# Kernel optimization log

Hardware: AMD Instinct MI355X
Metric: run time of the kernel (lower is better)

The kernel has to match this reference:

```python
import jax, jax.numpy as jnp
import numpy as np

EMBD = 512
HEADS = 8
HEAD = EMBD // HEADS


def setup_inputs() -> dict:
    key = jax.random.key(0)
    ks = jax.random.split(key, 9)
    B, M = 4, 2048
    s = 1.0 / np.sqrt(EMBD)
    inp = {
        "x": jax.random.normal(ks[0], (B, M, EMBD), dtype=jnp.float32),
        "wq": jax.random.uniform(ks[1], (EMBD, EMBD), jnp.float32, -s, s),
        "bq": jnp.zeros((EMBD,), jnp.float32),
        "wk": jax.random.uniform(ks[2], (EMBD, EMBD), jnp.float32, -s, s),
        "bk": jnp.zeros((EMBD,), jnp.float32),
        "wv": jax.random.uniform(ks[3], (EMBD, EMBD), jnp.float32, -s, s),
        "bv": jnp.zeros((EMBD,), jnp.float32),
        "wo": jax.random.uniform(ks[4], (EMBD, EMBD), jnp.float32, -s, s),
        "bo": jnp.zeros((EMBD,), jnp.float32),
        "gamma": jnp.ones((EMBD,), jnp.float32),
        "beta": jnp.zeros((EMBD,), jnp.float32),
    }
    return inp


def layer_norm(x, gamma, beta, eps=1e-5):
    mu = jnp.mean(x, axis=-1, keepdims=True)
    var = jnp.mean(jnp.square(x - mu), axis=-1, keepdims=True)
    return (x - mu) * jax.lax.rsqrt(var + eps) * gamma + beta


def reference(x, wq, bq, wk, bk, wv, bv, wo, bo, gamma, beta):
    B, M, _ = x.shape
    norm = layer_norm(x, gamma, beta)
    # projections; reshape to [B, H, M, Dh]
    def proj(w, b):
        return (norm @ w.T + b).reshape(B, M, HEADS, HEAD).transpose(0, 2, 1, 3)
    q = proj(wq, bq)
    k = proj(wk, bk)
    v = proj(wv, bv)
    scores = jnp.einsum("bhmd,bhnd->bhmn", q, k) / np.sqrt(HEAD)
    # exclude self-attention on the diagonal
    diag = jnp.eye(M, dtype=bool)
    scores = jnp.where(diag, -jnp.inf, scores)
    attn = jax.nn.softmax(scores, axis=-1)
    ctx = jnp.einsum("bhmn,bhnd->bhmd", attn, v)
    ctx = ctx.transpose(0, 2, 1, 3).reshape(B, M, EMBD)
    out = ctx @ wo.T + bo
    return (out + x, attn)
```

## Files before the change

kernel.cpp:

```cpp
#include <hip/hip_runtime.h>

#define B_   4
#define H_   8
#define M_   2048
#define D_   512
#define DH_  64

typedef short  bf16x8 __attribute__((ext_vector_type(8)));
typedef float  f32x4  __attribute__((ext_vector_type(4)));
typedef unsigned short u16x4 __attribute__((ext_vector_type(4)));

#define EXPC 0.18033688011112042f

static __device__ __forceinline__ unsigned short f2bf(float f) {
  unsigned u = __float_as_uint(f);
  u += 0x7fffu + ((u >> 16) & 1u);
  return (unsigned short)(u >> 16);
}

static __device__ __forceinline__ int swz128(int row, int byteoff) {
  return row * 128 + (byteoff ^ ((row & 7) << 4));
}

static __device__ __forceinline__ void glds16(const void* g, void* l) {
  __builtin_amdgcn_global_load_lds(
      (const __attribute__((address_space(1))) unsigned*)g,
      (__attribute__((address_space(3))) unsigned*)l, 16, 0, 0);
}

static __device__ __forceinline__ void stage_tile(
    const char* g0, size_t rstride, char* lds, int t) {
  const int r0 = t >> 3, c0 = t & 7;
  const char* src = g0 + (size_t)r0 * rstride + ((c0 ^ (r0 & 7)) << 4);
  char* dst = lds + ((t & 192) << 4);
  #pragma unroll
  for (int c = 0; c < 4; ++c)
    glds16(src + (size_t)c * 32 * rstride, dst + c * 4096);
}

__global__ __launch_bounds__(256) void ln_kernel(
    const float* __restrict__ x, const float* __restrict__ gamma,
    const float* __restrict__ beta, unsigned short* __restrict__ xn)
{
  int row = blockIdx.x;
  int t = threadIdx.x;
  const float* xr = x + (size_t)row * D_;
  float v0 = xr[t], v1 = xr[t + 256];
  float s = v0 + v1, ss = v0 * v0 + v1 * v1;
  #pragma unroll
  for (int m = 1; m < 64; m <<= 1) {
    s  += __shfl_xor(s, m);
    ss += __shfl_xor(ss, m);
  }
  __shared__ float red[8];
  int wid = t >> 6;
  if ((t & 63) == 0) { red[wid] = s; red[wid + 4] = ss; }
  __syncthreads();
  s  = red[0] + red[1] + red[2] + red[3];
  ss = red[4] + red[5] + red[6] + red[7];
  float mu  = s * (1.0f / D_);
  float var = ss * (1.0f / D_) - mu * mu;
  float rstd = rsqrtf(var + 1e-5f);
  unsigned short* o = xn + (size_t)row * D_;
  o[t]       = f2bf((v0 - mu) * rstd * gamma[t]       + beta[t]);
  o[t + 256] = f2bf((v1 - mu) * rstd * gamma[t + 256] + beta[t + 256]);
}

__global__ __launch_bounds__(256) void cast_w_kernel(
    const float* __restrict__ wq, const float* __restrict__ wk,
    const float* __restrict__ wv, const float* __restrict__ wo,
    unsigned short* __restrict__ wqkv, unsigned short* __restrict__ wob)
{
  int i = blockIdx.x * 256 + threadIdx.x;
  wqkv[i]          = f2bf(wq[i]);
  wqkv[i + 262144] = f2bf(wk[i]);
  wqkv[i + 524288] = f2bf(wv[i]);
  wob[i]           = f2bf(wo[i]);
}

__global__ __launch_bounds__(256) void qkv_gemm(
    const unsigned short* __restrict__ xn,
    const unsigned short* __restrict__ wqkv,
    const float* __restrict__ bq, const float* __restrict__ bk,
    const float* __restrict__ bv,
    unsigned short* __restrict__ q, unsigned short* __restrict__ k,
    unsigned short* __restrict__ vT)
{
  __shared__ __align__(16) char As[128 * 128];
  __shared__ __align__(16) char Bs[128 * 128];
  const int m0 = blockIdx.x * 128;
  const int n0 = blockIdx.y * 128;
  const int t = threadIdx.x, wid = t >> 6, lane = t & 63;
  const int wr = (wid >> 1) * 64, wc = (wid & 1) * 64;
  const int cl = lane & 15, rg = lane >> 4;
  const f32x4 z4 = {0.f, 0.f, 0.f, 0.f};
  const bool isv = (n0 >= 1024);

  const char* agb = (const char*)xn   + (size_t)m0 * 1024;
  const char* bgb = (const char*)wqkv + (size_t)n0 * 1024;

  f32x4 acc[4][4];
  #pragma unroll
  for (int i = 0; i < 4; ++i)
    #pragma unroll
    for (int j = 0; j < 4; ++j) acc[i][j] = z4;

  for (int k0 = 0; k0 < 512; k0 += 64) {
    __syncthreads();
    stage_tile(agb + k0 * 2, 1024, As, t);
    stage_tile(bgb + k0 * 2, 1024, Bs, t);
    __syncthreads();
    #pragma unroll
    for (int ks = 0; ks < 2; ++ks) {
      int koff = ks * 64 + rg * 16;
      bf16x8 af[4], bfr[4];
      #pragma unroll
      for (int i = 0; i < 4; ++i)
        af[i] = *(const bf16x8*)(As + swz128(wr + i * 16 + cl, koff));
      #pragma unroll
      for (int j = 0; j < 4; ++j)
        bfr[j] = *(const bf16x8*)(Bs + swz128(wc + j * 16 + cl, koff));
      if (isv) {
        #pragma unroll
        for (int i = 0; i < 4; ++i)
          #pragma unroll
          for (int j = 0; j < 4; ++j)
            acc[i][j] = __builtin_amdgcn_mfma_f32_16x16x32_bf16(af[i], bfr[j], acc[i][j], 0, 0, 0);
      } else {
        #pragma unroll
        for (int j = 0; j < 4; ++j)
          #pragma unroll
          for (int i = 0; i < 4; ++i)
            acc[j][i] = __builtin_amdgcn_mfma_f32_16x16x32_bf16(bfr[j], af[i], acc[j][i], 0, 0, 0);
      }
    }
  }

  if (isv) {
    #pragma unroll
    for (int j = 0; j < 4; ++j) {
      int n = n0 + wc + j * 16 + cl;
      int nn = n & 511;
      int h = nn >> 6, dh = nn & 63;
      float bias = bv[nn];
      #pragma unroll
      for (int i = 0; i < 4; ++i) {
        int mrow = m0 + wr + i * 16 + rg * 4;
        int b = mrow >> 11, mm = mrow & 2047;
        u16x4 u;
        #pragma unroll
        for (int r = 0; r < 4; ++r) u[r] = f2bf(acc[i][j][r] + bias);
        *(u16x4*)(vT + ((size_t)(b * H_ + h) * DH_ + dh) * M_ + mm) = u;
      }
    }
  } else {
    const int mat = n0 >> 9;
    unsigned short* dst = mat ? k : q;
    const float* bias = mat ? bk : bq;
    #pragma unroll
    for (int j = 0; j < 4; ++j) {
      int nn0 = ((n0 + wc) & 511) + j * 16 + rg * 4;
      int h = nn0 >> 6, dh = nn0 & 63;
      f32x4 b4 = *(const f32x4*)(bias + nn0);
      #pragma unroll
      for (int i = 0; i < 4; ++i) {
        int mrow = m0 + wr + i * 16 + cl;
        int b = mrow >> 11, mm = mrow & 2047;
        u16x4 u;
        #pragma unroll
        for (int r = 0; r < 4; ++r) u[r] = f2bf(acc[j][i][r] + b4[r]);
        *(u16x4*)(dst + ((size_t)(b * H_ + h) * M_ + mm) * DH_ + dh) = u;
      }
    }
  }
}

__global__ __launch_bounds__(256, 8) void psum_kernel(
    const unsigned short* __restrict__ q, const unsigned short* __restrict__ k,
    float* __restrict__ rinv)
{
  __shared__ __align__(16) char Kb[2][8192];
  const int flat = blockIdx.x;
  const int bh = (flat & 7) * 4 + ((flat >> 3) >> 5);
  const int mb = (flat >> 3) & 31;
  const int m0 = mb * 64;
  const int t = threadIdx.x, wid = t >> 6, lane = t & 63;
  const int wr = wid * 16, cl = lane & 15, rg = lane >> 4;
  const char* qb = (const char*)(q + (size_t)bh * M_ * DH_);
  const char* kb = (const char*)(k + (size_t)bh * M_ * DH_);
  const int m_g = m0 + wr + cl;
  const f32x4 z4 = {0.f, 0.f, 0.f, 0.f};

  bf16x8 qf[2];
  #pragma unroll
  for (int ks = 0; ks < 2; ++ks)
    qf[ks] = *(const bf16x8*)(qb + (size_t)m_g * 128 + ks * 64 + rg * 16);

  const int r0 = t >> 3, c0 = t & 7;
  const int ldsoff = (t & 192) * 16;
  const size_t sK0 = (size_t)r0 * 128 + ((c0 ^ (r0 & 7)) << 4);

  glds16(kb + sK0,        Kb[0] + ldsoff);
  glds16(kb + sK0 + 4096, Kb[0] + ldsoff + 4096);

  float psum = 0.f;
  int buf = 0;
  for (int nt = 0; nt < 32; ++nt) {
    __syncthreads();
    if (nt + 1 < 32) {
      const char* src = kb + (size_t)(nt + 1) * 8192;
      glds16(src + sK0,        Kb[buf ^ 1] + ldsoff);
      glds16(src + sK0 + 4096, Kb[buf ^ 1] + ldsoff + 4096);
    }
    f32x4 s[4];
    #pragma unroll
    for (int j = 0; j < 4; ++j) s[j] = z4;
    #pragma unroll
    for (int ks = 0; ks < 2; ++ks)
      #pragma unroll
      for (int j = 0; j < 4; ++j) {
        bf16x8 kf = *(const bf16x8*)(Kb[buf] + swz128(j * 16 + cl, ks * 64 + rg * 16));
        s[j] = __builtin_amdgcn_mfma_f32_16x16x32_bf16(kf, qf[ks], s[j], 0, 0, 0);
      }
    if (nt == mb) {
      #pragma unroll
      for (int j = 0; j < 4; ++j)
        #pragma unroll
        for (int r = 0; r < 4; ++r) {
          int n_g = nt * 64 + j * 16 + rg * 4 + r;
          float p = __builtin_amdgcn_exp2f(s[j][r] * EXPC);
          psum += (n_g == m_g) ? 0.f : p;
        }
    } else {
      #pragma unroll
      for (int j = 0; j < 4; ++j)
        #pragma unroll
        for (int r = 0; r < 4; ++r)
          psum += __builtin_amdgcn_exp2f(s[j][r] * EXPC);
    }
    buf ^= 1;
  }
  psum += __shfl_xor(psum, 16);
  psum += __shfl_xor(psum, 32);
  if (lane < 16) rinv[bh * M_ + m_g] = 1.0f / psum;
}

__global__ __launch_bounds__(256, 4) void attn_kernel(
    const unsigned short* __restrict__ q,
    const unsigned short* __restrict__ k,
    const unsigned short* __restrict__ vT,
    const float* __restrict__ rinv,
    float* __restrict__ attn,
    unsigned short* __restrict__ ctx)
{
  __shared__ __align__(16) char Kb[2][8192];
  __shared__ __align__(16) char Vb[2][8192];
  __shared__ __align__(16) char Ps[4][2048];

  const int flat = blockIdx.x;
  const int bh = (flat & 7) * 4 + ((flat >> 3) >> 5);
  const int mb = (flat >> 3) & 31;
  const int m0 = mb * 64;
  const int t = threadIdx.x, wid = t >> 6, lane = t & 63;
  const int wr = wid * 16, cl = lane & 15, rg = lane >> 4;
  const int m_g = m0 + wr + cl;
  const f32x4 z4 = {0.f, 0.f, 0.f, 0.f};

  const char* qb = (const char*)(q  + (size_t)bh * M_ * DH_);
  const char* kb = (const char*)(k  + (size_t)bh * M_ * DH_);
  const char* vb = (const char*)(vT + (size_t)bh * DH_ * M_);
  float* ab = attn + (size_t)bh * M_ * M_;

  const float rv = rinv[bh * M_ + m_g];
  bf16x8 qf[2];
  #pragma unroll
  for (int ks = 0; ks < 2; ++ks)
    qf[ks] = *(const bf16x8*)(qb + (size_t)m_g * 128 + ks * 64 + rg * 16);

  const int r0 = t >> 3, c0 = t & 7;
  const int ldsoff = (t & 192) * 16;
  const size_t sK0 = (size_t)r0 * 128 + ((c0 ^ (r0 & 7)) << 4);
  const size_t sV0 = (size_t)r0 * (M_ * 2) + ((c0 ^ (r0 & 7)) << 4);

  glds16(kb + sK0,                    Kb[0] + ldsoff);
  glds16(kb + sK0 + 4096,             Kb[0] + ldsoff + 4096);
  glds16(vb + sV0,                    Vb[0] + ldsoff);
  glds16(vb + sV0 + 32 * (M_ * 2),    Vb[0] + ldsoff + 4096);
  __syncthreads();

  f32x4 oc[4];
  #pragma unroll
  for (int j = 0; j < 4; ++j) oc[j] = z4;

  const int srow = lane >> 4;
  const int sch  = lane & 15;

  int buf = 0;
  for (int nt = 0; nt < 32; ++nt) {
    if (nt + 1 < 32) {
      const char* srcK = kb + (size_t)(nt + 1) * 8192;
      const char* srcV = vb + (size_t)(nt + 1) * 128;
      glds16(srcK + sK0,                 Kb[buf ^ 1] + ldsoff);
      glds16(srcK + sK0 + 4096,          Kb[buf ^ 1] + ldsoff + 4096);
      glds16(srcV + sV0,                 Vb[buf ^ 1] + ldsoff);
      glds16(srcV + sV0 + 32 * (M_ * 2), Vb[buf ^ 1] + ldsoff + 4096);
    }
    f32x4 s[4];
    #pragma unroll
    for (int j = 0; j < 4; ++j) s[j] = z4;
    #pragma unroll
    for (int ks = 0; ks < 2; ++ks)
      #pragma unroll
      for (int j = 0; j < 4; ++j) {
        bf16x8 kf = *(const bf16x8*)(Kb[buf] + swz128(j * 16 + cl, ks * 64 + rg * 16));
        s[j] = __builtin_amdgcn_mfma_f32_16x16x32_bf16(kf, qf[ks], s[j], 0, 0, 0);
      }
    const bool dtile = (nt == mb);
    #pragma unroll
    for (int j = 0; j < 4; ++j) {
      u16x4 u;
      #pragma unroll
      for (int r = 0; r < 4; ++r) {
        int n_g = nt * 64 + j * 16 + rg * 4 + r;
        float p = __builtin_amdgcn_exp2f(s[j][r] * EXPC) * rv;
        u[r] = f2bf((dtile && n_g == m_g) ? 0.f : p);
      }
      *(u16x4*)(Ps[wid] + swz128(cl, j * 32 + rg * 8)) = u;
    }
    {
      float* abase = ab + ((size_t)(m0 + wr + srow)) * M_ + nt * 64 + sch * 4;
      #pragma unroll
      for (int it = 0; it < 4; ++it) {
        u16x4 pu = *(const u16x4*)(Ps[wid] + swz128(it * 4 + srow, sch * 8));
        f32x4 pv;
        #pragma unroll
        for (int r = 0; r < 4; ++r) pv[r] = __uint_as_float((unsigned)pu[r] << 16);
        __builtin_nontemporal_store(pv, (f32x4*)(abase + (size_t)it * 4 * M_));
      }
    }
    #pragma unroll
    for (int ks = 0; ks < 2; ++ks) {
      bf16x8 pf = *(const bf16x8*)(Ps[wid] + swz128(cl, ks * 64 + rg * 16));
      #pragma unroll
      for (int jd = 0; jd < 4; ++jd) {
        bf16x8 vf = *(const bf16x8*)(Vb[buf] + swz128(jd * 16 + cl, ks * 64 + rg * 16));
        oc[jd] = __builtin_amdgcn_mfma_f32_16x16x32_bf16(vf, pf, oc[jd], 0, 0, 0);
      }
    }
    if (nt + 1 < 32) {
      asm volatile("s_waitcnt vmcnt(4) lgkmcnt(0)" ::: "memory");
      __builtin_amdgcn_s_barrier();
    }
    buf ^= 1;
  }

  int b = bh >> 3, h = bh & 7;
  unsigned short* crow = ctx + ((size_t)b * M_ + m_g) * D_ + h * DH_ + rg * 4;
  #pragma unroll
  for (int jd = 0; jd < 4; ++jd) {
    u16x4 u;
    #pragma unroll
    for (int r = 0; r < 4; ++r) u[r] = f2bf(oc[jd][r]);
    *(u16x4*)(crow + jd * 16) = u;
  }
}

__global__ __launch_bounds__(256) void out_gemm(
    const unsigned short* __restrict__ ctxb,
    const unsigned short* __restrict__ wob,
    const float* __restrict__ bo,
    const float* __restrict__ x,
    float* __restrict__ out)
{
  __shared__ __align__(16) char As[128 * 128];
  __shared__ __align__(16) char Bs[128 * 128];
  const int m0 = blockIdx.x * 128;
  const int n0 = blockIdx.y * 128;
  const int t = threadIdx.x, wid = t >> 6, lane = t & 63;
  const int wr = (wid >> 1) * 64, wc = (wid & 1) * 64;
  const int cl = lane & 15, rg = lane >> 4;
  const f32x4 z4 = {0.f, 0.f, 0.f, 0.f};

  const char* agb = (const char*)ctxb + (size_t)m0 * 1024;
  const char* bgb = (const char*)wob  + (size_t)n0 * 1024;

  f32x4 acc[4][4];
  #pragma unroll
  for (int j = 0; j < 4; ++j)
    #pragma unroll
    for (int i = 0; i < 4; ++i) acc[j][i] = z4;

  for (int k0 = 0; k0 < 512; k0 += 64) {
    __syncthreads();
    stage_tile(agb + k0 * 2, 1024, As, t);
    stage_tile(bgb + k0 * 2, 1024, Bs, t);
    __syncthreads();
    #pragma unroll
    for (int ks = 0; ks < 2; ++ks) {
      int koff = ks * 64 + rg * 16;
      bf16x8 af[4], bfr[4];
      #pragma unroll
      for (int i = 0; i < 4; ++i)
        af[i] = *(const bf16x8*)(As + swz128(wr + i * 16 + cl, koff));
      #pragma unroll
      for (int j = 0; j < 4; ++j)
        bfr[j] = *(const bf16x8*)(Bs + swz128(wc + j * 16 + cl, koff));
      #pragma unroll
      for (int j = 0; j < 4; ++j)
        #pragma unroll
        for (int i = 0; i < 4; ++i)
          acc[j][i] = __builtin_amdgcn_mfma_f32_16x16x32_bf16(bfr[j], af[i], acc[j][i], 0, 0, 0);
    }
  }

  #pragma unroll
  for (int j = 0; j < 4; ++j) {
    int nb = n0 + wc + j * 16 + rg * 4;
    f32x4 bo4 = *(const f32x4*)(bo + nb);
    #pragma unroll
    for (int i = 0; i < 4; ++i) {
      int m = m0 + wr + i * 16 + cl;
      f32x4 x4 = *(const f32x4*)(x + (size_t)m * 512 + nb);
      f32x4 o;
      #pragma unroll
      for (int r = 0; r < 4; ++r) o[r] = acc[j][i][r] + bo4[r] + x4[r];
      *(f32x4*)(out + (size_t)m * 512 + nb) = o;
    }
  }
}

extern "C" void kernel_launch(void* const* d_in, const int* in_sizes, int n_in,
                              void* d_out, int out_size, void* d_ws, size_t ws_size,
                              hipStream_t stream) {
  const float* x     = (const float*)d_in[0];
  const float* wq    = (const float*)d_in[1];
  const float* bq    = (const float*)d_in[2];
  const float* wk    = (const float*)d_in[3];
  const float* bk    = (const float*)d_in[4];
  const float* wv    = (const float*)d_in[5];
  const float* bv    = (const float*)d_in[6];
  const float* wo    = (const float*)d_in[7];
  const float* bo    = (const float*)d_in[8];
  const float* gamma = (const float*)d_in[9];
  const float* beta  = (const float*)d_in[10];

  char* ws = (char*)d_ws;
  unsigned short* xn   = (unsigned short*)(ws);
  unsigned short* wqkv = (unsigned short*)(ws + 8388608);
  float*          rinv = (float*)(ws + 8388608);
  unsigned short* wob  = (unsigned short*)(ws + 9961472);
  unsigned short* qb   = (unsigned short*)(ws + 10485760);
  unsigned short* kb   = (unsigned short*)(ws + 18874368);
  unsigned short* vT   = (unsigned short*)(ws + 27262976);
  unsigned short* ctx  = (unsigned short*)(ws + 35651584);

  float* out  = (float*)d_out;
  float* attn = (float*)d_out + 4194304;

  ln_kernel<<<8192, 256, 0, stream>>>(x, gamma, beta, xn);
  cast_w_kernel<<<1024, 256, 0, stream>>>(wq, wk, wv, wo, wqkv, wob);
  qkv_gemm<<<dim3(64, 12), 256, 0, stream>>>(xn, wqkv, bq, bk, bv, qb, kb, vT);
  psum_kernel<<<1024, 256, 0, stream>>>(qb, kb, rinv);
  attn_kernel<<<1024, 256, 0, stream>>>(qb, kb, vT, rinv, attn, ctx);
  out_gemm<<<dim3(64, 4), 256, 0, stream>>>(ctx, wob, bo, x, out);
}
```

Before: 214.1 us.

## Fuse row-sum pass into attention kernel, load V directly from global

Merges the separate softmax row-sum kernel into the attention kernel as a first pass over K, so the reciprocal stays in a register and no rinv buffer or extra launch is needed. V tiles are now read straight from global memory into registers instead of being staged through double-buffered LDS. The attn stores switch from nontemporal to regular stores, and the hand-written waitcnt/barrier is replaced with __syncthreads. This removes a kernel launch and frees LDS, at the cost of uncoalesced, register-heavy V loads and different cache behaviour for the large attn output write.

```diff
diff --git a/kernel.cpp b/kernel.cpp
--- a/kernel.cpp
+++ b/kernel.cpp
@@ -175,86 +175,14 @@
   }
 }
 
-__global__ __launch_bounds__(256, 8) void psum_kernel(
-    const unsigned short* __restrict__ q, const unsigned short* __restrict__ k,
-    float* __restrict__ rinv)
-{
-  __shared__ __align__(16) char Kb[2][8192];
-  const int flat = blockIdx.x;
-  const int bh = (flat & 7) * 4 + ((flat >> 3) >> 5);
-  const int mb = (flat >> 3) & 31;
-  const int m0 = mb * 64;
-  const int t = threadIdx.x, wid = t >> 6, lane = t & 63;
-  const int wr = wid * 16, cl = lane & 15, rg = lane >> 4;
-  const char* qb = (const char*)(q + (size_t)bh * M_ * DH_);
-  const char* kb = (const char*)(k + (size_t)bh * M_ * DH_);
-  const int m_g = m0 + wr + cl;
-  const f32x4 z4 = {0.f, 0.f, 0.f, 0.f};
-
-  bf16x8 qf[2];
-  #pragma unroll
-  for (int ks = 0; ks < 2; ++ks)
-    qf[ks] = *(const bf16x8*)(qb + (size_t)m_g * 128 + ks * 64 + rg * 16);
-
-  const int r0 = t >> 3, c0 = t & 7;
-  const int ldsoff = (t & 192) * 16;
-  const size_t sK0 = (size_t)r0 * 128 + ((c0 ^ (r0 & 7)) << 4);
-
-  glds16(kb + sK0,        Kb[0] + ldsoff);
-  glds16(kb + sK0 + 4096, Kb[0] + ldsoff + 4096);
-
-  float psum = 0.f;
-  int buf = 0;
-  for (int nt = 0; nt < 32; ++nt) {
-    __syncthreads();
-    if (nt + 1 < 32) {
-      const char* src = kb + (size_t)(nt + 1) * 8192;
-      glds16(src + sK0,        Kb[buf ^ 1] + ldsoff);
-      glds16(src + sK0 + 4096, Kb[buf ^ 1] + ldsoff + 4096);
-    }
-    f32x4 s[4];
-    #pragma unroll
-    for (int j = 0; j < 4; ++j) s[j] = z4;
-    #pragma unroll
-    for (int ks = 0; ks < 2; ++ks)
-      #pragma unroll
-      for (int j = 0; j < 4; ++j) {
-        bf16x8 kf = *(const bf16x8*)(Kb[buf] + swz128(j * 16 + cl, ks * 64 + rg * 16));
-        s[j] = __builtin_amdgcn_mfma_f32_16x16x32_bf16(kf, qf[ks], s[j], 0, 0, 0);
-      }
-    if (nt == mb) {
-      #pragma unroll
-      for (int j = 0; j < 4; ++j)
-        #pragma unroll
-        for (int r = 0; r < 4; ++r) {
-          int n_g = nt * 64 + j * 16 + rg * 4 + r;
-          float p = __builtin_amdgcn_exp2f(s[j][r] * EXPC);
-          psum += (n_g == m_g) ? 0.f : p;
-        }
-    } else {
-      #pragma unroll
-      for (int j = 0; j < 4; ++j)
-        #pragma unroll
-        for (int r = 0; r < 4; ++r)
-          psum += __builtin_amdgcn_exp2f(s[j][r] * EXPC);
-    }
-    buf ^= 1;
-  }
-  psum += __shfl_xor(psum, 16);
-  psum += __shfl_xor(psum, 32);
-  if (lane < 16) rinv[bh * M_ + m_g] = 1.0f / psum;
-}
-
 __global__ __launch_bounds__(256, 4) void attn_kernel(
     const unsigned short* __restrict__ q,
     const unsigned short* __restrict__ k,
     const unsigned short* __restrict__ vT,
-    const float* __restrict__ rinv,
     float* __restrict__ attn,
     unsigned short* __restrict__ ctx)
 {
   __shared__ __align__(16) char Kb[2][8192];
-  __shared__ __align__(16) char Vb[2][8192];
   __shared__ __align__(16) char Ps[4][2048];
 
   const int flat = blockIdx.x;
@@ -271,7 +199,6 @@
   const char* vb = (const char*)(vT + (size_t)bh * DH_ * M_);
   float* ab = attn + (size_t)bh * M_ * M_;
 
-  const float rv = rinv[bh * M_ + m_g];
   bf16x8 qf[2];
   #pragma unroll
   for (int ks = 0; ks < 2; ++ks)
@@ -280,31 +207,76 @@
   const int r0 = t >> 3, c0 = t & 7;
   const int ldsoff = (t & 192) * 16;
   const size_t sK0 = (size_t)r0 * 128 + ((c0 ^ (r0 & 7)) << 4);
-  const size_t sV0 = (size_t)r0 * (M_ * 2) + ((c0 ^ (r0 & 7)) << 4);
-
-  glds16(kb + sK0,                    Kb[0] + ldsoff);
-  glds16(kb + sK0 + 4096,             Kb[0] + ldsoff + 4096);
-  glds16(vb + sV0,                    Vb[0] + ldsoff);
-  glds16(vb + sV0 + 32 * (M_ * 2),    Vb[0] + ldsoff + 4096);
+
+  glds16(kb + sK0,        Kb[0] + ldsoff);
+  glds16(kb + sK0 + 4096, Kb[0] + ldsoff + 4096);
   __syncthreads();
 
-  f32x4 oc[4];
-  #pragma unroll
-  for (int j = 0; j < 4; ++j) oc[j] = z4;
-
-  const int srow = lane >> 4;
-  const int sch  = lane & 15;
-
+  float psum = 0.f;
   int buf = 0;
   for (int nt = 0; nt < 32; ++nt) {
     if (nt + 1 < 32) {
-      const char* srcK = kb + (size_t)(nt + 1) * 8192;
-      const char* srcV = vb + (size_t)(nt + 1) * 128;
-      glds16(srcK + sK0,                 Kb[buf ^ 1] + ldsoff);
-      glds16(srcK + sK0 + 4096,          Kb[buf ^ 1] + ldsoff + 4096);
-      glds16(srcV + sV0,                 Vb[buf ^ 1] + ldsoff);
-      glds16(srcV + sV0 + 32 * (M_ * 2), Vb[buf ^ 1] + ldsoff + 4096);
-    }
+      const char* src = kb + (size_t)(nt + 1) * 8192;
+      glds16(src + sK0,        Kb[buf ^ 1] + ldsoff);
+      glds16(src + sK0 + 4096, Kb[buf ^ 1] + ldsoff + 4096);
+    }
+    f32x4 s[4];
+    #pragma unroll
+    for (int j = 0; j < 4; ++j) s[j] = z4;
+    #pragma unroll
+    for (int ks = 0; ks < 2; ++ks)
+      #pragma unroll
+      for (int j = 0; j < 4; ++j) {
+        bf16x8 kf = *(const bf16x8*)(Kb[buf] + swz128(j * 16 + cl, ks * 64 + rg * 16));
+        s[j] = __builtin_amdgcn_mfma_f32_16x16x32_bf16(kf, qf[ks], s[j], 0, 0, 0);
+      }
+    if (nt == mb) {
+      #pragma unroll
+      for (int j = 0; j < 4; ++j)
+        #pragma unroll
+        for (int r = 0; r < 4; ++r) {
+          int n_g = nt * 64 + j * 16 + rg * 4 + r;
+          float p = __builtin_amdgcn_exp2f(s[j][r] * EXPC);
+          psum += (n_g == m_g) ? 0.f : p;
+        }
+    } else {
+      #pragma unroll
+      for (int j = 0; j < 4; ++j)
+        #pragma unroll
+        for (int r = 0; r < 4; ++r)
+          psum += __builtin_amdgcn_exp2f(s[j][r] * EXPC);
+    }
+    __syncthreads();
+    buf ^= 1;
+  }
+  psum += __shfl_xor(psum, 16);
+  psum += __shfl_xor(psum, 32);
+  const float rv = 1.0f / psum;
+
+  glds16(kb + sK0,        Kb[buf] + ldsoff);
+  glds16(kb + sK0 + 4096, Kb[buf] + ldsoff + 4096);
+  __syncthreads();
+
+  f32x4 oc[4];
+  #pragma unroll
+  for (int j = 0; j < 4; ++j) oc[j] = z4;
+
+  const int srow = lane >> 4;
+  const int sch  = lane & 15;
+
+  for (int nt = 0; nt < 32; ++nt) {
+    if (nt + 1 < 32) {
+      const char* src = kb + (size_t)(nt + 1) * 8192;
+      glds16(src + sK0,        Kb[buf ^ 1] + ldsoff);
+      glds16(src + sK0 + 4096, Kb[buf ^ 1] + ldsoff + 4096);
+    }
+    bf16x8 vf[8];
+    #pragma unroll
+    for (int jd = 0; jd < 4; ++jd)
+      #pragma unroll
+      for (int ks = 0; ks < 2; ++ks)
+        vf[jd * 2 + ks] = *(const bf16x8*)(
+            vb + (size_t)(jd * 16 + cl) * (M_ * 2) + nt * 128 + ks * 64 + rg * 16);
     f32x4 s[4];
     #pragma unroll
     for (int j = 0; j < 4; ++j) s[j] = z4;
@@ -335,22 +307,17 @@
         f32x4 pv;
         #pragma unroll
         for (int r = 0; r < 4; ++r) pv[r] = __uint_as_float((unsigned)pu[r] << 16);
-        __builtin_nontemporal_store(pv, (f32x4*)(abase + (size_t)it * 4 * M_));
+        *(f32x4*)(abase + (size_t)it * 4 * M_) = pv;
       }
     }
     #pragma unroll
     for (int ks = 0; ks < 2; ++ks) {
       bf16x8 pf = *(const bf16x8*)(Ps[wid] + swz128(cl, ks * 64 + rg * 16));
       #pragma unroll
-      for (int jd = 0; jd < 4; ++jd) {
-        bf16x8 vf = *(const bf16x8*)(Vb[buf] + swz128(jd * 16 + cl, ks * 64 + rg * 16));
-        oc[jd] = __builtin_amdgcn_mfma_f32_16x16x32_bf16(vf, pf, oc[jd], 0, 0, 0);
-      }
-    }
-    if (nt + 1 < 32) {
-      asm volatile("s_waitcnt vmcnt(4) lgkmcnt(0)" ::: "memory");
-      __builtin_amdgcn_s_barrier();
-    }
+      for (int jd = 0; jd < 4; ++jd)
+        oc[jd] = __builtin_amdgcn_mfma_f32_16x16x32_bf16(vf[jd * 2 + ks], pf, oc[jd], 0, 0, 0);
+    }
+    __syncthreads();
     buf ^= 1;
   }
 
@@ -447,7 +414,6 @@
   char* ws = (char*)d_ws;
   unsigned short* xn   = (unsigned short*)(ws);
   unsigned short* wqkv = (unsigned short*)(ws + 8388608);
-  float*          rinv = (float*)(ws + 8388608);
   unsigned short* wob  = (unsigned short*)(ws + 9961472);
   unsigned short* qb   = (unsigned short*)(ws + 10485760);
   unsigned short* kb   = (unsigned short*)(ws + 18874368);
@@ -460,7 +426,6 @@
   ln_kernel<<<8192, 256, 0, stream>>>(x, gamma, beta, xn);
   cast_w_kernel<<<1024, 256, 0, stream>>>(wq, wk, wv, wo, wqkv, wob);
   qkv_gemm<<<dim3(64, 12), 256, 0, stream>>>(xn, wqkv, bq, bk, bv, qb, kb, vT);
-  psum_kernel<<<1024, 256, 0, stream>>>(qb, kb, rinv);
-  attn_kernel<<<1024, 256, 0, stream>>>(qb, kb, vT, rinv, attn, ctx);
+  attn_kernel<<<1024, 256, 0, stream>>>(qb, kb, vT, attn, ctx);
   out_gemm<<<dim3(64, 4), 256, 0, stream>>>(ctx, wob, bo, x, out);
 }
```

Result: slower. 284.6 us (+32.9%).
